# Optimization experiments

Measured on AMD Instinct MI355X. Metric: run time of the kernel, lower is better.

The kernel has to match this reference:

```python
import jax, jax.numpy as jnp
import numpy as np

N, E, FD, PD, C0, C1 = 50000, 1000000, 1024, 64, 64, 64


def setup_inputs() -> dict:
    key = jax.random.key(0)
    ks = iter(jax.random.split(key, 64))
    nrm = lambda s, sc=0.05: jax.random.normal(next(ks), s, jnp.float32) * sc

    def bn_p(c):
        # rows: gamma, beta, running_mean, running_var (eval-mode batchnorm)
        return jnp.stack([
            1.0 + 0.1 * jax.random.normal(next(ks), (c,)),
            0.1 * jax.random.normal(next(ks), (c,)),
            0.1 * jax.random.normal(next(ks), (c,)),
            0.5 + jax.random.uniform(next(ks), (c,)),
        ]).astype(jnp.float32)

    inp = {}
    inp["x"] = jax.random.normal(next(ks), (N, FD + 4), jnp.float32)
    inp["edge_index"] = jax.random.randint(next(ks), (2, E), 0, N, jnp.int32)
    inp["edge_attr"] = jax.random.randint(next(ks), (E,), 0, 3, jnp.int32) - 1  # {-1,0,1}
    inp["Wspf"] = nrm((PD, 4)); inp["bspf"] = nrm((PD,))
    inp["W011"] = nrm((C0, FD // 2 + PD)); inp["b011"] = nrm((C0,))
    inp["W012"] = nrm((C0, FD // 2)); inp["b012"] = nrm((C0,))
    inp["bn01"] = bn_p(C0)
    for i in (1, 2, 3):
        inp[f"e{i}W1"] = nrm((C0, 2 * C0)); inp[f"e{i}b1"] = nrm((C0,))
        inp[f"e{i}W2"] = nrm((C0, C0)); inp[f"e{i}b2"] = nrm((C0,))
        inp[f"bn1{i}"] = bn_p(C0)
    inp["s21Wl"] = nrm((C1, C0)); inp["s21bl"] = nrm((C1,)); inp["s21Wr"] = nrm((C1, C0))
    inp["bn21"] = bn_p(C1)
    for i in (1, 2, 3):
        inp[f"s3{i}Wl"] = nrm((1, C1)); inp[f"s3{i}bl"] = nrm((1,)); inp[f"s3{i}Wr"] = nrm((1, C1))
    return inp


def _bn(h, p):
    g, b, m, v = p
    return (h - m) * jax.lax.rsqrt(v + 1e-5) * g + b


def _edge_conv(h, src, dst, seg, n, W1, b1, W2, b2):
    # EdgeConv: max_j MLP([x_i, x_j - x_i]); masked edges routed to dummy segment n
    xi, xj = h[dst], h[src]
    msg = jax.nn.relu(jnp.concatenate([xi, xj - xi], axis=1) @ W1.T + b1) @ W2.T + b2
    out = jax.ops.segment_max(msg, seg, num_segments=n + 1)[:n]
    return jnp.where(jnp.isfinite(out), out, 0.0)  # nodes with no in-edges -> 0


def _sage(h, src, seg, n, Wl, bl, Wr):
    # SAGEConv: lin_l(mean_j x_j) + lin_r(x_i)
    s = jax.ops.segment_sum(h[src], seg, num_segments=n + 1)[:n]
    cnt = jax.ops.segment_sum(jnp.ones((seg.shape[0],), h.dtype), seg, num_segments=n + 1)[:n]
    agg = s / jnp.maximum(cnt, 1.0)[:, None]
    return agg @ Wl.T + bl + h @ Wr.T


def reference(x, edge_index, edge_attr, Wspf, bspf, W011, b011, W012, b012, bn01,
              e1W1, e1b1, e1W2, e1b2, bn11, e2W1, e2b1, e2W2, e2b2, bn12,
              e3W1, e3b1, e3W2, e3b2, bn13, s21Wl, s21bl, s21Wr, bn21,
              s31Wl, s31bl, s31Wr, s32Wl, s32bl, s32Wr, s33Wl, s33bl, s33Wr):
    fd = 1024
    n = x.shape[0]
    src, dst = edge_index[0], edge_index[1]
    seg1 = jnp.where(edge_attr >= 0, dst, n)  # forward-time edges
    seg2 = jnp.where(edge_attr <= 0, dst, n)  # backward-time edges
    seg3 = dst                                 # all edges

    spf = x[:, fd:fd + 4]
    x_vis = jnp.concatenate([x[:, fd // 2:fd], spf @ Wspf.T + bspf], axis=1) @ W011.T + b011
    x_aud = x[:, :fd // 2] @ W012.T + b012
    h = jax.nn.relu(_bn(x_aud + x_vis, bn01))

    def branch(eW1, eb1, eW2, eb2, bnE, seg, sWl, sbl, sWr):
        y = jax.nn.relu(_bn(_edge_conv(h, src, dst, seg, n, eW1, eb1, eW2, eb2), bnE))
        y = jax.nn.relu(_bn(_sage(y, src, seg, n, s21Wl, s21bl, s21Wr), bn21))
        return _sage(y, src, seg, n, sWl, sbl, sWr)

    o = (branch(e1W1, e1b1, e1W2, e1b2, bn11, seg1, s31Wl, s31bl, s31Wr)
         + branch(e2W1, e2b1, e2W2, e2b2, bn12, seg2, s32Wl, s32bl, s32Wr)
         + branch(e3W1, e3b1, e3W2, e3b2, bn13, seg3, s33Wl, s33bl, s33Wr))
    return jax.nn.sigmoid(o)
```

## Files before the change

### kernel.cpp

```cpp
#include <hip/hip_runtime.h>
#include <cstdint>
#include <cstddef>

#define NN 50000
#define EE 1000000
#define NBK 196
#define PW_EC 6144
#define PW_AG 8192

typedef __attribute__((ext_vector_type(8))) short bf16x8;
typedef __attribute__((ext_vector_type(4))) short s16x4;
typedef __attribute__((ext_vector_type(4))) float f32x4;
typedef _Float16 f16;
typedef __attribute__((ext_vector_type(2))) _Float16 f16x2;
typedef __attribute__((ext_vector_type(4))) _Float16 f16x4;
typedef __attribute__((ext_vector_type(8))) _Float16 f16x8;

__device__ __forceinline__ void split2(float v, short& hi, short& lo) {
    union { float f; unsigned int u; } a; a.f = v;
    unsigned short h16 = (unsigned short)(a.u >> 16);
    union { unsigned int u; float f; } hf; hf.u = ((unsigned int)h16) << 16;
    union { float f; unsigned int u; } b; b.f = v - hf.f;
    hi = (short)h16;
    lo = (short)(b.u >> 16);
}

__device__ __forceinline__ f16x8 relupq(f16x8 p, f16x8 q) {
    f16x8 s = p + q;
    f16x8 z = {};
#if __has_builtin(__builtin_elementwise_max)
    return __builtin_elementwise_max(s, z);
#else
    f16x8 r;
#pragma unroll
    for (int j = 0; j < 8; j++) r[j] = (s[j] > (f16)0.f) ? s[j] : (f16)0.f;
    return r;
#endif
}

#define OFF_WHL    ((size_t)0)
#define OFF_WSPP   ((size_t)262144)
#define OFF_BIAS01 ((size_t)263168)
#define OFF_W1PQT  ((size_t)263424)
#define OFF_BIASPQ ((size_t)361728)
#define OFF_WSAGET ((size_t)363264)
#define OFF_BIAS21 ((size_t)396032)
#define OFF_BNF    ((size_t)396288)
#define OFF_W2BF   ((size_t)398848)
#define OFF_INVC4  ((size_t)423424)
#define OFF_PZ4    ((size_t)1223424)
#define OFF_RP     ((size_t)2023424)
#define OFF_PARTS  ((size_t)2223488)
#define OFF_DEG    ((size_t)2227584)
#define OFF_CNT01  ((size_t)2427648)
#define OFF_GHEAD  ((size_t)2627712)
#define OFF_SORT   ((size_t)2631808)
#define OFF_H      ((size_t)6631808)
#define OFF_PI     ((size_t)19431808)
#define OFF_QI     ((size_t)38631808)
#define OFF_Y1I    ((size_t)57831808)
#define OFF_EBUCK  OFF_H
#define OFF_AGGI   OFF_PI

__global__ __launch_bounds__(256) void k_prep(
    const float* __restrict__ Wspf, const float* __restrict__ bspf,
    const float* __restrict__ W011, const float* __restrict__ b011,
    const float* __restrict__ W012, const float* __restrict__ b012,
    const float* __restrict__ bn01,
    const float* __restrict__ e1W1, const float* __restrict__ e1b1,
    const float* __restrict__ e1b2, const float* __restrict__ bn11,
    const float* __restrict__ e2W1, const float* __restrict__ e2b1,
    const float* __restrict__ e2b2, const float* __restrict__ bn12,
    const float* __restrict__ e3W1, const float* __restrict__ e3b1,
    const float* __restrict__ e3b2, const float* __restrict__ bn13,
    const float* __restrict__ e1W2, const float* __restrict__ e2W2,
    const float* __restrict__ e3W2,
    const float* __restrict__ s21Wl, const float* __restrict__ s21bl,
    const float* __restrict__ s21Wr, const float* __restrict__ bn21,
    unsigned short* __restrict__ Whl, float* __restrict__ WspP, float* __restrict__ bias01,
    float* __restrict__ W1pqT, float* __restrict__ biasPQ,
    float* __restrict__ WsageT, float* __restrict__ bias21, float* __restrict__ bnf,
    f16* __restrict__ W2h)
{
    int idx = blockIdx.x * 256 + threadIdx.x;
    if (idx < 131072) {
        int hl = idx >> 16;
        int r = idx & 65535;
        int kchunk = r >> 11;
        int r2 = r & 2047;
        int blk = r2 >> 9;
        int r3 = r2 & 511;
        int lane = r3 >> 3;
        int j = r3 & 7;
        int n = lane & 15, quad = lane >> 4;
        int k = kchunk * 32 + quad * 8 + j;
        int c = blk * 16 + n;
        float s = bn01[c] * rsqrtf(bn01[192 + c] + 1e-5f);
        float w = ((k < 512) ? W012[c * 512 + k] : W011[c * 576 + (k - 512)]) * s;
        short hi, lo;
        split2(w, hi, lo);
        Whl[idx] = (unsigned short)(hl ? lo : hi);
    } else if (idx < 131072 + 24576) {
        int r = idx - 131072;
        int b = r >> 13; r &= 8191;
        int k = r >> 7, cp = r & 127;
        const float* W1 = (b == 0) ? e1W1 : (b == 1) ? e2W1 : e3W1;
        float val;
        if (cp < 64) val = W1[cp * 128 + k] - W1[cp * 128 + 64 + k];
        else         val = W1[(cp - 64) * 128 + 64 + k];
        W1pqT[b * 8192 + k * 128 + cp] = val;
    } else if (idx < 131072 + 24576 + 8192) {
        int r = idx - (131072 + 24576);
        int k = r >> 6, c = r & 63;
        float s = bn21[c] * rsqrtf(bn21[192 + c] + 1e-5f);
        float w = (k < 64) ? s21Wl[c * 64 + k] : s21Wr[c * 64 + (k - 64)];
        WsageT[k * 64 + c] = w * s;
    } else if (idx < 131072 + 24576 + 8192 + 64) {
        int c = idx - (131072 + 24576 + 8192);
        float s01 = bn01[c] * rsqrtf(bn01[192 + c] + 1e-5f);
        float wsp0 = 0.f, wsp1 = 0.f, wsp2 = 0.f, wsp3 = 0.f, bacc = 0.f;
        for (int j = 0; j < 64; j++) {
            float w = W011[c * 576 + 512 + j];
            wsp0 += w * Wspf[j * 4 + 0];
            wsp1 += w * Wspf[j * 4 + 1];
            wsp2 += w * Wspf[j * 4 + 2];
            wsp3 += w * Wspf[j * 4 + 3];
            bacc += w * bspf[j];
        }
        WspP[c * 4 + 0] = wsp0 * s01; WspP[c * 4 + 1] = wsp1 * s01;
        WspP[c * 4 + 2] = wsp2 * s01; WspP[c * 4 + 3] = wsp3 * s01;
        bias01[c] = (b011[c] + b012[c] + bacc) * s01 + (bn01[64 + c] - bn01[128 + c] * s01);
        float s21 = bn21[c] * rsqrtf(bn21[192 + c] + 1e-5f);
        bias21[c] = s21bl[c] * s21 + (bn21[64 + c] - bn21[128 + c] * s21);
        const float* b1a[3] = { e1b1, e2b1, e3b1 };
        const float* b2a[3] = { e1b2, e2b2, e3b2 };
        const float* bna[3] = { bn11, bn12, bn13 };
#pragma unroll
        for (int b = 0; b < 3; b++) {
            float s = bna[b][c] * rsqrtf(bna[b][192 + c] + 1e-5f);
            float tr = bna[b][64 + c] - bna[b][128 + c] * s;
            bnf[b * 192 + c] = s;
            bnf[b * 192 + 64 + c] = b2a[b][c] * s + tr;
            bnf[b * 192 + 128 + c] = tr;
            biasPQ[b * 128 + c] = b1a[b][c];
            biasPQ[b * 128 + 64 + c] = 0.f;
        }
    } else if (idx < 131072 + 24576 + 8192 + 64 + 12288) {
        int r = idx - (131072 + 24576 + 8192 + 64);
        int b = r >> 12, i = r & 4095;
        const float* W2 = (b == 0) ? e1W2 : (b == 1) ? e2W2 : e3W2;
        W2h[b * 4096 + i] = (f16)W2[i];
    }
}

__global__ __launch_bounds__(256) void k_hist(
    const int* __restrict__ dst, int* __restrict__ deg)
{
    int e = blockIdx.x * 256 + threadIdx.x;
    if (e < EE) atomicAdd(&deg[dst[e]], 1);
}

__global__ __launch_bounds__(256) void k_psum(const int* __restrict__ deg, int* __restrict__ parts)
{
    int i = blockIdx.x * 256 + threadIdx.x;
    int v = (i < NN) ? deg[i] : 0;
#pragma unroll
    for (int off = 32; off > 0; off >>= 1) v += __shfl_xor(v, off);
    __shared__ int ws4[4];
    int wid = threadIdx.x >> 6;
    if ((threadIdx.x & 63) == 0) ws4[wid] = v;
    __syncthreads();
    if (threadIdx.x == 0)
        parts[blockIdx.x] = ws4[0] + ws4[1] + ws4[2] + ws4[3];
}

__global__ __launch_bounds__(256) void k_pscan(int* __restrict__ parts, int* __restrict__ ghead)
{
    __shared__ int sbuf[256];
    int tid = threadIdx.x;
    int v = (tid < NBK) ? parts[tid] : 0;
    sbuf[tid] = v;
    __syncthreads();
    for (int off = 1; off < 256; off <<= 1) {
        int t = (tid >= off) ? sbuf[tid - off] : 0;
        __syncthreads();
        sbuf[tid] += t;
        __syncthreads();
    }
    if (tid < NBK) {
        int ex = sbuf[tid] - v;
        parts[tid] = ex;
        ghead[tid] = ex;
    }
}

__global__ __launch_bounds__(256) void k_scanfix(
    const int* __restrict__ deg, const int* __restrict__ parts, int* __restrict__ rowptr)
{
    __shared__ int sbuf[256];
    int tid = threadIdx.x;
    int i = blockIdx.x * 256 + tid;
    int v = (i < NN) ? deg[i] : 0;
    sbuf[tid] = v;
    __syncthreads();
    for (int off = 1; off < 256; off <<= 1) {
        int t = (tid >= off) ? sbuf[tid - off] : 0;
        __syncthreads();
        sbuf[tid] += t;
        __syncthreads();
    }
    int base = parts[blockIdx.x];
    if (i < NN)      rowptr[i] = base + sbuf[tid] - v;
    if (i == NN - 1) rowptr[NN] = base + sbuf[tid];
}

__global__ __launch_bounds__(256) void k_bucketA(
    const int* __restrict__ src, const int* __restrict__ dst, const int* __restrict__ attr,
    int* __restrict__ ghead, unsigned int* __restrict__ ebuck)
{
    __shared__ int hist[NBK];
    __shared__ int head[NBK];
    int tid = threadIdx.x;
    if (tid < NBK) hist[tid] = 0;
    __syncthreads();
    int base_e = blockIdx.x * 4096;
    unsigned int word[16]; int bkt[16];
#pragma unroll
    for (int k = 0; k < 16; k++) {
        int e = base_e + k * 256 + tid;
        if (e < EE) {
            int d = dst[e], s = src[e], a = attr[e] + 1;
            int b = d >> 8;
            word[k] = (unsigned)s | ((unsigned)a << 16) | ((unsigned)(d & 255) << 18);
            bkt[k] = b;
            atomicAdd(&hist[b], 1);
        } else { bkt[k] = -1; word[k] = 0; }
    }
    __syncthreads();
    if (tid < NBK) {
        int c = hist[tid];
        head[tid] = c ? atomicAdd(&ghead[tid], c) : 0;
    }
    __syncthreads();
#pragma unroll
    for (int k = 0; k < 16; k++) {
        if (bkt[k] >= 0) {
            int pos = atomicAdd(&head[bkt[k]], 1);
            ebuck[pos] = word[k];
        }
    }
}

__global__ __launch_bounds__(256) void k_bucketB(
    const int* __restrict__ rp, const unsigned int* __restrict__ ebuck,
    int* __restrict__ sorted, unsigned int* __restrict__ cnt01)
{
    __shared__ int sbuf[1024];
    __shared__ int head[1024];
    __shared__ int s2[256];
    int b = blockIdx.x, tid = threadIdx.x;
    int n0 = b * 256;
    int n1 = n0 + 256; if (n1 > NN) n1 = NN;
    int r0 = rp[n0];
    int r1 = rp[n1];
    for (int i = tid; i < 1024; i += 256) sbuf[i] = 0;
    __syncthreads();
    for (int e = r0 + tid; e < r1; e += 256)
        atomicAdd(&sbuf[(ebuck[e] >> 16) & 1023], 1);
    __syncthreads();
    int i0 = tid * 4;
    int v0 = sbuf[i0], v1 = sbuf[i0 + 1], v2 = sbuf[i0 + 2], v3 = sbuf[i0 + 3];
    if (n0 + tid < NN)
        cnt01[n0 + tid] = (unsigned)v0 | ((unsigned)v1 << 16);
    int tot = v0 + v1 + v2 + v3;
    s2[tid] = tot;
    __syncthreads();
    for (int off = 1; off < 256; off <<= 1) {
        int t = (tid >= off) ? s2[tid - off] : 0;
        __syncthreads();
        s2[tid] += t;
        __syncthreads();
    }
    int ex = s2[tid] - tot;
    head[i0]     = r0 + ex;
    head[i0 + 1] = r0 + ex + v0;
    head[i0 + 2] = r0 + ex + v0 + v1;
    head[i0 + 3] = r0 + ex + v0 + v1 + v2;
    __syncthreads();
    for (int e = r0 + tid; e < r1; e += 256) {
        unsigned int w = ebuck[e];
        int pos = atomicAdd(&head[(w >> 16) & 1023], 1);
        sorted[pos] = (int)(w & 0x3FFFFu);
    }
}

__global__ __launch_bounds__(256) void k_h(
    const float* __restrict__ x, const unsigned short* __restrict__ Whl,
    const float* __restrict__ WspP, const float* __restrict__ bias01,
    float* __restrict__ h)
{
    __shared__ unsigned short hib[2][4096];
    __shared__ unsigned short lob[2][4096];
    int tid = threadIdx.x;
    int w = tid >> 6, l = tid & 63;
    int tile = blockIdx.x;
    int m = l & 15, quad = l >> 4;
    int blk = w;
    const unsigned short* Wh = Whl;
    const unsigned short* Wl = Whl + 65536;
    const size_t xbase = (size_t)tile * 16 * 1028;

    int oct_w = l >> 1, off_w = (l & 1) * 4;

    f32x4 g[4];
#pragma unroll
    for (int p = 0; p < 4; p++)
        g[p] = *(const f32x4*)(x + xbase + (size_t)(p * 4 + w) * 1028 + l * 4);
#pragma unroll
    for (int p = 0; p < 4; p++) {
        int r = p * 4 + w;
        int op = r * 256 + (oct_w ^ (r & 7)) * 8 + off_w;
        s16x4 h4, l4;
#pragma unroll
        for (int i = 0; i < 4; i++) { short hi, lo; split2(g[p][i], hi, lo); h4[i] = hi; l4[i] = lo; }
        *(s16x4*)(&hib[0][op]) = h4;
        *(s16x4*)(&lob[0][op]) = l4;
    }
    __syncthreads();

    f32x4 acc = { 0.f, 0.f, 0.f, 0.f };
    for (int c = 0; c < 4; c++) {
        if (c < 3) {
#pragma unroll
            for (int p = 0; p < 4; p++)
                g[p] = *(const f32x4*)(x + xbase + (size_t)(p * 4 + w) * 1028 + (c + 1) * 256 + l * 4);
        }
        int buf = c & 1;
        const unsigned short* hp = &hib[buf][m * 256];
        const unsigned short* lp = &lob[buf][m * 256];
        int msw = m & 7;
#pragma unroll
        for (int ks = 0; ks < 8; ks++) {
            int oct = ks * 4 + quad;
            int ao = (oct ^ msw) * 8;
            bf16x8 xh = *(const bf16x8*)(hp + ao);
            bf16x8 xl = *(const bf16x8*)(lp + ao);
            int fb = (c * 8 + ks) * 2048 + blk * 512 + l * 8;
            bf16x8 bh = *(const bf16x8*)(Wh + fb);
            bf16x8 bl = *(const bf16x8*)(Wl + fb);
            acc = __builtin_amdgcn_mfma_f32_16x16x32_bf16(xh, bh, acc, 0, 0, 0);
            acc = __builtin_amdgcn_mfma_f32_16x16x32_bf16(xl, bh, acc, 0, 0, 0);
            acc = __builtin_amdgcn_mfma_f32_16x16x32_bf16(xh, bl, acc, 0, 0, 0);
        }
        if (c < 3) {
            int nbuf = (c + 1) & 1;
#pragma unroll
            for (int p = 0; p < 4; p++) {
                int r = p * 4 + w;
                int op = r * 256 + (oct_w ^ (r & 7)) * 8 + off_w;
                s16x4 h4, l4;
#pragma unroll
                for (int i = 0; i < 4; i++) { short hi, lo; split2(g[p][i], hi, lo); h4[i] = hi; l4[i] = lo; }
                *(s16x4*)(&hib[nbuf][op]) = h4;
                *(s16x4*)(&lob[nbuf][op]) = l4;
            }
            __syncthreads();
        }
    }

    int ch = blk * 16 + m;
    f32x4 wsp = *(const f32x4*)(WspP + ch * 4);
    float bia = bias01[ch];
#pragma unroll
    for (int r = 0; r < 4; r++) {
        int row = tile * 16 + quad * 4 + r;
        f32x4 sp = *(const f32x4*)(x + (size_t)row * 1028 + 1024);
        float a = acc[r] + sp[0] * wsp[0] + sp[1] * wsp[1]
                + sp[2] * wsp[2] + sp[3] * wsp[3] + bia;
        h[(size_t)row * 64 + ch] = fmaxf(a, 0.f);
    }
}

__global__ __launch_bounds__(256) void k_pq(
    const float* __restrict__ h, const float* __restrict__ WT3,
    const float* __restrict__ biasPQ, f16* __restrict__ Pi, f16* __restrict__ Qi)
{
    __shared__ float wt[64 * 128];
    __shared__ float xt[64 * 68];
    int tid = threadIdx.x;
    int m0 = blockIdx.x * 64;
    int cg = tid & 31, rg = tid >> 5;
#pragma unroll
    for (int i = 0; i < 4; i++) {
        int li = i * 256 + tid;
        int rr = li >> 4, q = li & 15;
        int row = m0 + rr;
        float4 u = make_float4(0.f, 0.f, 0.f, 0.f);
        if (row < NN) u = *(const float4*)(h + (size_t)row * 64 + q * 4);
        *(float4*)(xt + rr * 68 + q * 4) = u;
    }
    for (int b = 0; b < 3; b++) {
        __syncthreads();
#pragma unroll
        for (int i = 0; i < 8; i++)
            ((float4*)wt)[i * 256 + tid] = ((const float4*)(WT3 + b * 8192))[i * 256 + tid];
        __syncthreads();
        float acc[8][4];
#pragma unroll
        for (int r = 0; r < 8; r++)
#pragma unroll
            for (int j = 0; j < 4; j++) acc[r][j] = 0.f;
#pragma unroll 8
        for (int k = 0; k < 64; k++) {
            float4 wv = *(const float4*)(wt + k * 128 + cg * 4);
#pragma unroll
            for (int r = 0; r < 8; r++) {
                float xv = xt[(rg * 8 + r) * 68 + k];
                acc[r][0] += xv * wv.x; acc[r][1] += xv * wv.y;
                acc[r][2] += xv * wv.z; acc[r][3] += xv * wv.w;
            }
        }
        const float* biasP = biasPQ + b * 128;
#pragma unroll
        for (int r = 0; r < 8; r++) {
            int row = m0 + rg * 8 + r;
            if (row < NN) {
                if (cg < 16) {
                    f16x4 res;
#pragma unroll
                    for (int j = 0; j < 4; j++)
                        res[j] = (f16)(acc[r][j] + biasP[cg * 4 + j]);
                    *(f16x4*)(Pi + (size_t)row * 192 + b * 64 + cg * 4) = res;
                } else {
                    f16x4 res;
#pragma unroll
                    for (int j = 0; j < 4; j++)
                        res[j] = (f16)acc[r][j];
                    *(f16x4*)(Qi + (size_t)row * 192 + b * 64 + (cg - 16) * 4) = res;
                }
            }
        }
    }
}

#define ECV_BRANCH(B, EST, ECN)                                                    \
    {                                                                              \
        f16x8 pl = *(const f16x8*)(pr + (B) * 64 + quad * 8);                      \
        f16x8 ph = *(const f16x8*)(pr + (B) * 64 + 32 + quad * 8);                 \
        float acc[4][4];                                                           \
        _Pragma("unroll") for (int blk = 0; blk < 4; blk++)                        \
            _Pragma("unroll") for (int r = 0; r < 4; r++) acc[blk][r] = -3.0e38f;  \
        int nbF = (ECN) >> 4;                                                      \
        int rem = (ECN) & 15;                                                      \
        for (int bi = 0; bi < nbF; bi++) {                                         \
            int srcm = sorted[(EST) + bi * 16 + m] & 0xFFFF;                       \
            const f16* qr = Qi + (size_t)srcm * 192 + (B) * 64;                    \
            f16x8 q0 = *(const f16x8*)(qr + quad * 8);                             \
            f16x8 q1 = *(const f16x8*)(qr + 32 + quad * 8);                        \
            f16x8 a0 = relupq(pl, q0);                                             \
            f16x8 a1 = relupq(ph, q1);                                             \
            _Pragma("unroll") for (int blk = 0; blk < 4; blk++) {                  \
                f32x4 c = { 0.f, 0.f, 0.f, 0.f };                                  \
                f16x8 w0 = *(const f16x8*)(w2s + ((B) * 8 + blk * 2 + 0) * 512 + quad * 128 + m * 8); \
                f16x8 w1 = *(const f16x8*)(w2s + ((B) * 8 + blk * 2 + 1) * 512 + quad * 128 + m * 8); \
                c = __builtin_amdgcn_mfma_f32_16x16x32_f16(a0, w0, c, 0, 0, 0);    \
                c = __builtin_amdgcn_mfma_f32_16x16x32_f16(a1, w1, c, 0, 0, 0);    \
                _Pragma("unroll") for (int r = 0; r < 4; r++)                      \
                    acc[blk][r] = fmaxf(acc[blk][r], c[r]);                        \
            }                                                                      \
        }                                                                          \
        if (rem) {                                                                 \
            int e = (EST) + nbF * 16 + m;                                          \
            int srcm = sorted[(m < rem) ? e : (EST)] & 0xFFFF;                     \
            const f16* qr = Qi + (size_t)srcm * 192 + (B) * 64;                    \
            f16x8 q0 = *(const f16x8*)(qr + quad * 8);                             \
            f16x8 q1 = *(const f16x8*)(qr + 32 + quad * 8);                        \
            f16x8 a0 = relupq(pl, q0);                                             \
            f16x8 a1 = relupq(ph, q1);                                             \
            _Pragma("unroll") for (int blk = 0; blk < 4; blk++) {                  \
                f32x4 c = { 0.f, 0.f, 0.f, 0.f };                                  \
                f16x8 w0 = *(const f16x8*)(w2s + ((B) * 8 + blk * 2 + 0) * 512 + quad * 128 + m * 8); \
                f16x8 w1 = *(const f16x8*)(w2s + ((B) * 8 + blk * 2 + 1) * 512 + quad * 128 + m * 8); \
                c = __builtin_amdgcn_mfma_f32_16x16x32_f16(a0, w0, c, 0, 0, 0);    \
                c = __builtin_amdgcn_mfma_f32_16x16x32_f16(a1, w1, c, 0, 0, 0);    \
                _Pragma("unroll") for (int r = 0; r < 4; r++)                      \
                    if (quad * 4 + r < rem)                                        \
                        acc[blk][r] = fmaxf(acc[blk][r], c[r]);                    \
            }                                                                      \
        }                                                                          \
        float red[4];                                                              \
        _Pragma("unroll") for (int blk = 0; blk < 4; blk++) {                      \
            float rv = fmaxf(fmaxf(acc[blk][0], acc[blk][1]),                      \
                             fmaxf(acc[blk][2], acc[blk][3]));                     \
            rv = fmaxf(rv, __shfl_xor(rv, 16));                                    \
            rv = fmaxf(rv, __shfl_xor(rv, 32));                                    \
            red[blk] = rv;                                                         \
        }                                                                          \
        float mx = red[quad];                                                      \
        const float* scb = bnf + (B) * 192;                                        \
        float outv = ((ECN) > 0) ? fmaxf(fmaf(mx, scb[lane], scb[64 + lane]), 0.f) \
                                 : fmaxf(scb[128 + lane], 0.f);                    \
        y1i[(size_t)v * 192 + (B) * 64 + lane] = (f16)outv;                        \
    }

__global__ __launch_bounds__(256) void k_edgeconv_f(
    const int* __restrict__ rowptr, const unsigned int* __restrict__ cnt01,
    const int* __restrict__ sorted,
    const f16* __restrict__ Pi, const f16* __restrict__ Qi,
    const f16* __restrict__ W2h,
    const float* __restrict__ bnf,
    f16* __restrict__ y1i, float* __restrict__ invc4)
{
    __shared__ f16 w2s[12288];
    int tid = threadIdx.x;
#pragma unroll
    for (int u0 = 0; u0 < 6; u0++) {
        int u = u0 * 256 + tid;
        int frag = u >> 6;
        int rem = u & 63;
        int m2 = rem >> 2, qd = rem & 3;
        int bb = frag >> 3, blk = (frag >> 1) & 3, kc = frag & 1;
        *(int4*)(w2s + frag * 512 + qd * 128 + m2 * 8) =
            *(const int4*)(W2h + (bb * 64 + blk * 16 + m2) * 64 + kc * 32 + qd * 8);
    }
    __syncthreads();

    int wid = tid >> 6, lane = tid & 63;
    int m = lane & 15, quad = lane >> 4;
    int gw = blockIdx.x * 4 + wid;

    for (int v = gw; v < NN; v += PW_EC) {
        const f16* pr = Pi + (size_t)v * 192;
        int e0 = rowptr[v], e1 = rowptr[v + 1];
        int deg = e1 - e0;
        unsigned int cc = cnt01[v];
        int c0 = (int)(cc & 0xFFFFu);
        int c1 = (int)(cc >> 16);
        int n1cnt = deg - c0;
        int n2cnt = c0 + c1;

        ECV_BRANCH(0, e0 + c0, n1cnt)
        ECV_BRANCH(1, e0, n2cnt)
        ECV_BRANCH(2, e0, deg)

        if (lane == 0) {
            float4 ic;
            ic.x = 1.f / (float)(n1cnt > 0 ? n1cnt : 1);
            ic.y = 1.f / (float)(n2cnt > 0 ? n2cnt : 1);
            ic.z = 1.f / (float)(deg   > 0 ? deg   : 1);
            ic.w = 0.f;
            *(float4*)(invc4 + (size_t)v * 4) = ic;
        }
    }
}

#define AGG_BRANCH(B, EST, ECN, ICS)                                               \
    {                                                                              \
        float s[8];                                                                \
        _Pragma("unroll") for (int j = 0; j < 8; j++) s[j] = 0.f;                  \
        for (int eb = 0; eb < (ECN); eb += 8) {                                    \
            if (eb + eslot < (ECN)) {                                              \
                int src = sorted[(EST) + eb + eslot] & 0xFFFF;                     \
                f16x8 u = *(const f16x8*)(y1i + (size_t)src * 192 + (B) * 64 + cg * 8); \
                _Pragma("unroll") for (int j = 0; j < 8; j++) s[j] += (float)u[j]; \
            }                                                                      \
        }                                                                          \
        _Pragma("unroll") for (int j = 0; j < 8; j++) {                            \
            s[j] += __shfl_xor(s[j], 8);                                           \
            s[j] += __shfl_xor(s[j], 16);                                          \
            s[j] += __shfl_xor(s[j], 32);                                          \
        }                                                                          \
        if (eslot == 0) {                                                          \
            f16x8 r;                                                               \
            _Pragma("unroll") for (int j = 0; j < 8; j++) r[j] = (f16)(s[j] * (ICS)); \
            *(f16x8*)(aggi + (size_t)v * 192 + (B) * 64 + cg * 8) = r;             \
        }                                                                          \
    }

__global__ __launch_bounds__(256) void k_agg_f(
    const int* __restrict__ rowptr, const unsigned int* __restrict__ cnt01,
    const int* __restrict__ sorted,
    const f16* __restrict__ y1i, const float* __restrict__ invc4,
    f16* __restrict__ aggi)
{
    int wid = threadIdx.x >> 6, lane = threadIdx.x & 63;
    int eslot = lane >> 3, cg = lane & 7;
    int gw = blockIdx.x * 4 + wid;
    for (int v = gw; v < NN; v += PW_AG) {
        int e0 = rowptr[v], e1 = rowptr[v + 1];
        int deg = e1 - e0;
        unsigned int cc = cnt01[v];
        int c0 = (int)(cc & 0xFFFFu);
        int c1 = (int)(cc >> 16);
        float4 icv = *(const float4*)(invc4 + (size_t)v * 4);
        AGG_BRANCH(0, e0 + c0, deg - c0, icv.x)
        AGG_BRANCH(1, e0, c0 + c1, icv.y)
        AGG_BRANCH(2, e0, deg, icv.z)
    }
}

__global__ __launch_bounds__(256) void k_sage1(
    const f16* __restrict__ aggi, const f16* __restrict__ y1i,
    const float* __restrict__ WsageT, const float* __restrict__ bias21,
    const float* __restrict__ Wl0, const float* __restrict__ bl0, const float* __restrict__ Wr0,
    const float* __restrict__ Wl1, const float* __restrict__ bl1, const float* __restrict__ Wr1,
    const float* __restrict__ Wl2, const float* __restrict__ bl2, const float* __restrict__ Wr2,
    float* __restrict__ pz4)
{
    __shared__ float wt[64 * 64];
    __shared__ float xt[128 * 68];
    __shared__ float wl[64], wr[64];
    int tid = threadIdx.x;
    int m0 = blockIdx.x * 128;
    int cg = tid & 15, rg = tid >> 4;
    float zsum[8];
#pragma unroll
    for (int r = 0; r < 8; r++) zsum[r] = 0.f;

    for (int b = 0; b < 3; b++) {
        const float* Wl3 = (b == 0) ? Wl0 : (b == 1) ? Wl1 : Wl2;
        const float* bl3 = (b == 0) ? bl0 : (b == 1) ? bl1 : bl2;
        const float* Wr3 = (b == 0) ? Wr0 : (b == 1) ? Wr1 : Wr2;
        __syncthreads();
        if (tid < 64) { wl[tid] = Wl3[tid]; wr[tid] = Wr3[tid]; }
        float blv = bl3[0];
        float acc[8][4];
#pragma unroll
        for (int r = 0; r < 8; r++)
#pragma unroll
            for (int j = 0; j < 4; j++) acc[r][j] = 0.f;
        for (int ch = 0; ch < 2; ch++) {
            const f16* A = (ch ? y1i : aggi) + b * 64;
            __syncthreads();
#pragma unroll
            for (int i = 0; i < 4; i++)
                ((float4*)wt)[i * 256 + tid] = ((const float4*)(WsageT + ch * 4096))[i * 256 + tid];
#pragma unroll
            for (int i = 0; i < 4; i++) {
                int li = i * 256 + tid;
                int rr = li >> 3, q = li & 7;
                int row = m0 + rr;
                f16x8 u = {};
                if (row < NN) u = *(const f16x8*)(A + (size_t)row * 192 + q * 8);
                float4 lo4 = make_float4((float)u[0], (float)u[1], (float)u[2], (float)u[3]);
                float4 hi4 = make_float4((float)u[4], (float)u[5], (float)u[6], (float)u[7]);
                *(float4*)(xt + rr * 68 + q * 8) = lo4;
                *(float4*)(xt + rr * 68 + q * 8 + 4) = hi4;
            }
            __syncthreads();
#pragma unroll 8
            for (int k = 0; k < 64; k++) {
                float4 wv = *(const float4*)(wt + k * 64 + cg * 4);
#pragma unroll
                for (int r = 0; r < 8; r++) {
                    float xv = xt[(rg * 8 + r) * 68 + k];
                    acc[r][0] += xv * wv.x; acc[r][1] += xv * wv.y;
                    acc[r][2] += xv * wv.z; acc[r][3] += xv * wv.w;
                }
            }
        }
#pragma unroll
        for (int r = 0; r < 8; r++) {
            int row = m0 + rg * 8 + r;
            float ap = 0.f, az = 0.f;
#pragma unroll
            for (int j = 0; j < 4; j++) {
                float t = fmaxf(acc[r][j] + bias21[cg * 4 + j], 0.f);
                ap += t * wl[cg * 4 + j];
                az += t * wr[cg * 4 + j];
            }
            ap += __shfl_xor(ap, 1); ap += __shfl_xor(ap, 2);
            ap += __shfl_xor(ap, 4); ap += __shfl_xor(ap, 8);
            az += __shfl_xor(az, 1); az += __shfl_xor(az, 2);
            az += __shfl_xor(az, 4); az += __shfl_xor(az, 8);
            zsum[r] += az + blv;
            if (cg == 0 && row < NN)
                pz4[(size_t)row * 4 + b] = ap;
        }
    }
#pragma unroll
    for (int r = 0; r < 8; r++) {
        int row = m0 + rg * 8 + r;
        if (cg == 0 && row < NN)
            pz4[(size_t)row * 4 + 3] = zsum[r];
    }
}

__global__ __launch_bounds__(256) void k_sage2_f(
    const int* __restrict__ rowptr, const int* __restrict__ sorted,
    const float* __restrict__ pz4, const float* __restrict__ invc4,
    float* __restrict__ outp)
{
    int wid = threadIdx.x >> 6, lane = threadIdx.x & 63;
    int sub = lane >> 4, sl = lane & 15;
    int gw = blockIdx.x * 4 + wid;
    for (int v = gw * 4 + sub; v < NN; v += PW_AG * 4) {
        int e0 = rowptr[v], e1 = rowptr[v + 1];
        float s1 = 0.f, s2 = 0.f, s3 = 0.f;
        for (int e = e0 + sl; e < e1; e += 16) {
            int w = sorted[e];
            int src = w & 0xFFFF, a = (w >> 16) & 3;
            float4 pz = *(const float4*)(pz4 + (size_t)src * 4);
            s3 += pz.z;
            if (a >= 1) s1 += pz.x;
            if (a <= 1) s2 += pz.y;
        }
#pragma unroll
        for (int off = 1; off < 16; off <<= 1) {
            s1 += __shfl_xor(s1, off);
            s2 += __shfl_xor(s2, off);
            s3 += __shfl_xor(s3, off);
        }
        if (sl == 0) {
            float4 icv = *(const float4*)(invc4 + (size_t)v * 4);
            float zsum = pz4[(size_t)v * 4 + 3];
            float val = s1 * icv.x + s2 * icv.y + s3 * icv.z + zsum;
            outp[v] = 1.f / (1.f + expf(-val));
        }
    }
}

extern "C" void kernel_launch(void* const* d_in, const int* in_sizes, int n_in,
                              void* d_out, int out_size, void* d_ws, size_t ws_size,
                              hipStream_t stream)
{
    const float* x    = (const float*)d_in[0];
    const int* ei     = (const int*)d_in[1];
    const int* attr   = (const int*)d_in[2];
    const float* Wspf = (const float*)d_in[3];
    const float* bspf = (const float*)d_in[4];
    const float* W011 = (const float*)d_in[5];
    const float* b011 = (const float*)d_in[6];
    const float* W012 = (const float*)d_in[7];
    const float* b012 = (const float*)d_in[8];
    const float* bn01 = (const float*)d_in[9];
    const float* eW1[3] = { (const float*)d_in[10], (const float*)d_in[15], (const float*)d_in[20] };
    const float* eb1[3] = { (const float*)d_in[11], (const float*)d_in[16], (const float*)d_in[21] };
    const float* eW2[3] = { (const float*)d_in[12], (const float*)d_in[17], (const float*)d_in[22] };
    const float* eb2[3] = { (const float*)d_in[13], (const float*)d_in[18], (const float*)d_in[23] };
    const float* bn1[3] = { (const float*)d_in[14], (const float*)d_in[19], (const float*)d_in[24] };
    const float* s21Wl = (const float*)d_in[25];
    const float* s21bl = (const float*)d_in[26];
    const float* s21Wr = (const float*)d_in[27];
    const float* bn21  = (const float*)d_in[28];
    const float* s3Wl[3] = { (const float*)d_in[29], (const float*)d_in[32], (const float*)d_in[35] };
    const float* s3bl[3] = { (const float*)d_in[30], (const float*)d_in[33], (const float*)d_in[36] };
    const float* s3Wr[3] = { (const float*)d_in[31], (const float*)d_in[34], (const float*)d_in[37] };

    char* ws = (char*)d_ws;
    unsigned short* Whl = (unsigned short*)(ws + OFF_WHL);
    float* WspP   = (float*)(ws + OFF_WSPP);
    float* bias01 = (float*)(ws + OFF_BIAS01);
    float* W1pqT  = (float*)(ws + OFF_W1PQT);
    float* biasPQ = (float*)(ws + OFF_BIASPQ);
    float* WsageT = (float*)(ws + OFF_WSAGET);
    float* bias21 = (float*)(ws + OFF_BIAS21);
    float* bnf    = (float*)(ws + OFF_BNF);
    f16*   W2h    = (f16*)(ws + OFF_W2BF);
    float* invc4  = (float*)(ws + OFF_INVC4);
    float* pz4    = (float*)(ws + OFF_PZ4);
    int*   rp     = (int*)(ws + OFF_RP);
    int*   parts  = (int*)(ws + OFF_PARTS);
    int*   deg    = (int*)(ws + OFF_DEG);
    unsigned int* cnt01 = (unsigned int*)(ws + OFF_CNT01);
    int*   ghead  = (int*)(ws + OFF_GHEAD);
    int*   sorted = (int*)(ws + OFF_SORT);
    unsigned int* ebuck = (unsigned int*)(ws + OFF_EBUCK);
    float* h      = (float*)(ws + OFF_H);
    f16*   Pi     = (f16*)(ws + OFF_PI);
    f16*   Qi     = (f16*)(ws + OFF_QI);
    f16*   y1i    = (f16*)(ws + OFF_Y1I);
    f16*   aggi   = (f16*)(ws + OFF_AGGI);

    hipMemsetAsync(ws + OFF_DEG, 0, 200064, stream);

    k_prep<<<689, 256, 0, stream>>>(
        Wspf, bspf, W011, b011, W012, b012, bn01,
        eW1[0], eb1[0], eb2[0], bn1[0],
        eW1[1], eb1[1], eb2[1], bn1[1],
        eW1[2], eb1[2], eb2[2], bn1[2],
        eW2[0], eW2[1], eW2[2],
        s21Wl, s21bl, s21Wr, bn21,
        Whl, WspP, bias01, W1pqT, biasPQ, WsageT, bias21, bnf, W2h);

    k_hist<<<3907, 256, 0, stream>>>(ei + EE, deg);
    k_psum<<<NBK, 256, 0, stream>>>(deg, parts);
    k_pscan<<<1, 256, 0, stream>>>(parts, ghead);
    k_scanfix<<<NBK, 256, 0, stream>>>(deg, parts, rp);
    k_bucketA<<<245, 256, 0, stream>>>(ei, ei + EE, attr, ghead, ebuck);
    k_bucketB<<<NBK, 256, 0, stream>>>(rp, ebuck, sorted, cnt01);

    k_h<<<3125, 256, 0, stream>>>(x, Whl, WspP, bias01, h);

    k_pq<<<782, 256, 0, stream>>>(h, W1pqT, biasPQ, Pi, Qi);

    k_edgeconv_f<<<PW_EC / 4, 256, 0, stream>>>(rp, cnt01, sorted, Pi, Qi, W2h, bnf, y1i, invc4);
    k_agg_f<<<PW_AG / 4, 256, 0, stream>>>(rp, cnt01, sorted, y1i, invc4, aggi);

    k_sage1<<<391, 256, 0, stream>>>(aggi, y1i, WsageT, bias21,
                                     s3Wl[0], s3bl[0], s3Wr[0],
                                     s3Wl[1], s3bl[1], s3Wr[1],
                                     s3Wl[2], s3bl[2], s3Wr[2], pz4);

    k_sage2_f<<<PW_AG / 4, 256, 0, stream>>>(rp, sorted, pz4, invc4, (float*)d_out);
}
```

Before: 749.4 us.

## Rewrite SAGE layer-1 GEMM with fp16 MFMA and wave-per-16-row tiles

Replaces the scalar FP32 shared-memory GEMM in k_sage1 with 16x16x32 fp16 MFMA instructions. Each wave handles a 16-row tile and reads activations straight from global memory. The combined SAGE weights are now stored as fp16 in a padded LDS layout, and the grid doubles to match the new tiling. This removes most LDS traffic, the fp16-to-fp32 conversion and the scalar FMA work. The cost is fp16 weight rounding, which may change accuracy slightly.

New measurement: 711.4 us. -5.1%, faster.

```diff
diff --git a/kernel.cpp b/kernel.cpp
--- a/kernel.cpp
+++ b/kernel.cpp
@@ -7,6 +7,7 @@
 #define NBK 196
 #define PW_EC 6144
 #define PW_AG 8192
+#define SG_PAD 136
 
 typedef __attribute__((ext_vector_type(8))) short bf16x8;
 typedef __attribute__((ext_vector_type(4))) short s16x4;
@@ -79,7 +80,7 @@
     const float* __restrict__ s21Wr, const float* __restrict__ bn21,
     unsigned short* __restrict__ Whl, float* __restrict__ WspP, float* __restrict__ bias01,
     float* __restrict__ W1pqT, float* __restrict__ biasPQ,
-    float* __restrict__ WsageT, float* __restrict__ bias21, float* __restrict__ bnf,
+    f16* __restrict__ Wsg16, float* __restrict__ bias21, float* __restrict__ bnf,
     f16* __restrict__ W2h)
 {
     int idx = blockIdx.x * 256 + threadIdx.x;
@@ -114,7 +115,7 @@
         int k = r >> 6, c = r & 63;
         float s = bn21[c] * rsqrtf(bn21[192 + c] + 1e-5f);
         float w = (k < 64) ? s21Wl[c * 64 + k] : s21Wr[c * 64 + (k - 64)];
-        WsageT[k * 64 + c] = w * s;
+        Wsg16[c * 128 + k] = (f16)(w * s);
     } else if (idx < 131072 + 24576 + 8192 + 64) {
         int c = idx - (131072 + 24576 + 8192);
         float s01 = bn01[c] * rsqrtf(bn01[192 + c] + 1e-5f);
@@ -601,88 +602,81 @@
 
 __global__ __launch_bounds__(256) void k_sage1(
     const f16* __restrict__ aggi, const f16* __restrict__ y1i,
-    const float* __restrict__ WsageT, const float* __restrict__ bias21,
+    const f16* __restrict__ Wsg16,
+    const float* __restrict__ bias21,
     const float* __restrict__ Wl0, const float* __restrict__ bl0, const float* __restrict__ Wr0,
     const float* __restrict__ Wl1, const float* __restrict__ bl1, const float* __restrict__ Wr1,
     const float* __restrict__ Wl2, const float* __restrict__ bl2, const float* __restrict__ Wr2,
     float* __restrict__ pz4)
 {
-    __shared__ float wt[64 * 64];
-    __shared__ float xt[128 * 68];
-    __shared__ float wl[64], wr[64];
+    __shared__ f16 wsg[64 * SG_PAD];
     int tid = threadIdx.x;
-    int m0 = blockIdx.x * 128;
-    int cg = tid & 15, rg = tid >> 4;
-    float zsum[8];
-#pragma unroll
-    for (int r = 0; r < 8; r++) zsum[r] = 0.f;
-
+    for (int i = tid; i < 1024; i += 256) {
+        int c = i >> 4, kq = i & 15;
+        *(f16x8*)(wsg + c * SG_PAD + kq * 8) = *(const f16x8*)(Wsg16 + c * 128 + kq * 8);
+    }
+    __syncthreads();
+
+    int wid = tid >> 6, lane = tid & 63;
+    int m = lane & 15, quad = lane >> 4;
+    int tile = blockIdx.x * 4 + wid;
+    if (tile >= 3125) return;
+    int rowm = tile * 16 + m;
+    int rowq = tile * 16 + quad * 4;
+
+    const float* Wlp[3] = { Wl0, Wl1, Wl2 };
+    const float* Wrp[3] = { Wr0, Wr1, Wr2 };
+    const float* blp[3] = { bl0, bl1, bl2 };
+
+    float zsum[4] = { 0.f, 0.f, 0.f, 0.f };
+#pragma unroll
     for (int b = 0; b < 3; b++) {
-        const float* Wl3 = (b == 0) ? Wl0 : (b == 1) ? Wl1 : Wl2;
-        const float* bl3 = (b == 0) ? bl0 : (b == 1) ? bl1 : bl2;
-        const float* Wr3 = (b == 0) ? Wr0 : (b == 1) ? Wr1 : Wr2;
-        __syncthreads();
-        if (tid < 64) { wl[tid] = Wl3[tid]; wr[tid] = Wr3[tid]; }
-        float blv = bl3[0];
-        float acc[8][4];
-#pragma unroll
-        for (int r = 0; r < 8; r++)
-#pragma unroll
-            for (int j = 0; j < 4; j++) acc[r][j] = 0.f;
-        for (int ch = 0; ch < 2; ch++) {
-            const f16* A = (ch ? y1i : aggi) + b * 64;
-            __syncthreads();
-#pragma unroll
-            for (int i = 0; i < 4; i++)
-                ((float4*)wt)[i * 256 + tid] = ((const float4*)(WsageT + ch * 4096))[i * 256 + tid];
-#pragma unroll
-            for (int i = 0; i < 4; i++) {
-                int li = i * 256 + tid;
-                int rr = li >> 3, q = li & 7;
-                int row = m0 + rr;
-                f16x8 u = {};
-                if (row < NN) u = *(const f16x8*)(A + (size_t)row * 192 + q * 8);
-                float4 lo4 = make_float4((float)u[0], (float)u[1], (float)u[2], (float)u[3]);
-                float4 hi4 = make_float4((float)u[4], (float)u[5], (float)u[6], (float)u[7]);
-                *(float4*)(xt + rr * 68 + q * 8) = lo4;
-                *(float4*)(xt + rr * 68 + q * 8 + 4) = hi4;
+        const f16* ra = aggi + (size_t)rowm * 192 + b * 64 + quad * 8;
+        const f16* ry = y1i  + (size_t)rowm * 192 + b * 64 + quad * 8;
+        f16x8 a0 = *(const f16x8*)(ra);
+        f16x8 a1 = *(const f16x8*)(ra + 32);
+        f16x8 a2 = *(const f16x8*)(ry);
+        f16x8 a3 = *(const f16x8*)(ry + 32);
+        float ps[4] = { 0.f, 0.f, 0.f, 0.f };
+        float zs[4] = { 0.f, 0.f, 0.f, 0.f };
+#pragma unroll
+        for (int cb = 0; cb < 4; cb++) {
+            int col = cb * 16 + m;
+            const f16* wb = wsg + col * SG_PAD + quad * 8;
+            f32x4 acc = { 0.f, 0.f, 0.f, 0.f };
+            acc = __builtin_amdgcn_mfma_f32_16x16x32_f16(a0, *(const f16x8*)(wb),      acc, 0, 0, 0);
+            acc = __builtin_amdgcn_mfma_f32_16x16x32_f16(a1, *(const f16x8*)(wb + 32), acc, 0, 0, 0);
+            acc = __builtin_amdgcn_mfma_f32_16x16x32_f16(a2, *(const f16x8*)(wb + 64), acc, 0, 0, 0);
+            acc = __builtin_amdgcn_mfma_f32_16x16x32_f16(a3, *(const f16x8*)(wb + 96), acc, 0, 0, 0);
+            float bz = bias21[col];
+            float wlv = Wlp[b][col];
+            float wrv = Wrp[b][col];
+#pragma unroll
+            for (int r = 0; r < 4; r++) {
+                float y = fmaxf(acc[r] + bz, 0.f);
+                ps[r] += y * wlv;
+                zs[r] += y * wrv;
             }
-            __syncthreads();
-#pragma unroll 8
-            for (int k = 0; k < 64; k++) {
-                float4 wv = *(const float4*)(wt + k * 64 + cg * 4);
-#pragma unroll
-                for (int r = 0; r < 8; r++) {
-                    float xv = xt[(rg * 8 + r) * 68 + k];
-                    acc[r][0] += xv * wv.x; acc[r][1] += xv * wv.y;
-                    acc[r][2] += xv * wv.z; acc[r][3] += xv * wv.w;
-                }
-            }
-        }
-#pragma unroll
-        for (int r = 0; r < 8; r++) {
-            int row = m0 + rg * 8 + r;
-            float ap = 0.f, az = 0.f;
-#pragma unroll
-            for (int j = 0; j < 4; j++) {
-                float t = fmaxf(acc[r][j] + bias21[cg * 4 + j], 0.f);
-                ap += t * wl[cg * 4 + j];
-                az += t * wr[cg * 4 + j];
-            }
-            ap += __shfl_xor(ap, 1); ap += __shfl_xor(ap, 2);
-            ap += __shfl_xor(ap, 4); ap += __shfl_xor(ap, 8);
-            az += __shfl_xor(az, 1); az += __shfl_xor(az, 2);
-            az += __shfl_xor(az, 4); az += __shfl_xor(az, 8);
-            zsum[r] += az + blv;
-            if (cg == 0 && row < NN)
-                pz4[(size_t)row * 4 + b] = ap;
-        }
-    }
-#pragma unroll
-    for (int r = 0; r < 8; r++) {
-        int row = m0 + rg * 8 + r;
-        if (cg == 0 && row < NN)
-            pz4[(size_t)row * 4 + 3] = zsum[r];
+        }
+        float blv = blp[b][0];
+#pragma unroll
+        for (int r = 0; r < 4; r++) {
+            ps[r] += __shfl_xor(ps[r], 1); ps[r] += __shfl_xor(ps[r], 2);
+            ps[r] += __shfl_xor(ps[r], 4); ps[r] += __shfl_xor(ps[r], 8);
+            zs[r] += __shfl_xor(zs[r], 1); zs[r] += __shfl_xor(zs[r], 2);
+            zs[r] += __shfl_xor(zs[r], 4); zs[r] += __shfl_xor(zs[r], 8);
+            zsum[r] += zs[r] + blv;
+        }
+        if (m == 0) {
+#pragma unroll
+            for (int r = 0; r < 4; r++)
+                pz4[(size_t)(rowq + r) * 4 + b] = ps[r];
+        }
+    }
+    if (m == 0) {
+#pragma unroll
+        for (int r = 0; r < 4; r++)
+            pz4[(size_t)(rowq + r) * 4 + 3] = zsum[r];
     }
 }
 
@@ -753,7 +747,7 @@
     float* bias01 = (float*)(ws + OFF_BIAS01);
     float* W1pqT  = (float*)(ws + OFF_W1PQT);
     float* biasPQ = (float*)(ws + OFF_BIASPQ);
-    float* WsageT = (float*)(ws + OFF_WSAGET);
+    f16*   Wsg16  = (f16*)(ws + OFF_WSAGET);
     float* bias21 = (float*)(ws + OFF_BIAS21);
     float* bnf    = (float*)(ws + OFF_BNF);
     f16*   W2h    = (f16*)(ws + OFF_W2BF);
@@ -781,7 +775,7 @@
         eW1[2], eb1[2], eb2[2], bn1[2],
         eW2[0], eW2[1], eW2[2],
         s21Wl, s21bl, s21Wr, bn21,
-        Whl, WspP, bias01, W1pqT, biasPQ, WsageT, bias21, bnf, W2h);
+        Whl, WspP, bias01, W1pqT, biasPQ, Wsg16, bias21, bnf, W2h);
 
     k_hist<<<3907, 256, 0, stream>>>(ei + EE, deg);
     k_psum<<<NBK, 256, 0, stream>>>(deg, parts);
@@ -797,7 +791,7 @@
     k_edgeconv_f<<<PW_EC / 4, 256, 0, stream>>>(rp, cnt01, sorted, Pi, Qi, W2h, bnf, y1i, invc4);
     k_agg_f<<<PW_AG / 4, 256, 0, stream>>>(rp, cnt01, sorted, y1i, invc4, aggi);
 
-    k_sage1<<<391, 256, 0, stream>>>(aggi, y1i, WsageT, bias21,
+    k_sage1<<<782, 256, 0, stream>>>(aggi, y1i, Wsg16, bias21,
                                      s3Wl[0], s3bl[0], s3Wr[0],
                                      s3Wl[1], s3bl[1], s3Wr[1],
                                      s3Wl[2], s3bl[2], s3Wr[2], pz4);
```
